# Optimization experiments

Hardware: AMD Instinct MI355X
Metric: run time of the kernel (lower is better)

Reference implementation:

```python
import jax, jax.numpy as jnp
import numpy as np

N = 100000  # nodes
E = 3200000  # edges
NEG_SLOPE = 0.2  # GATConv default


def _gat_conv(x, src, dst, edge_attr, W, a_src, a_dst, W_e, a_e, bias):
    """PyG GATConv, heads=1, concat=True, add_self_loops=True (fill_value='mean')."""
    n = x.shape[0]
    loop = jnp.arange(n)
    s = jnp.concatenate([src, loop])
    d = jnp.concatenate([dst, loop])
    mean_ea = edge_attr.mean(axis=0)
    ea = jnp.concatenate([edge_attr, jnp.broadcast_to(mean_ea, (n, edge_attr.shape[1]))], axis=0)
    h = x @ W                          # [N, C]
    al_src = h @ a_src                 # [N]
    al_dst = h @ a_dst                 # [N]
    he = ea @ W_e                      # [E+N, C]
    alpha = al_src[s] + al_dst[d] + he @ a_e   # [E+N]
    alpha = jax.nn.leaky_relu(alpha, NEG_SLOPE)
    amax = jax.ops.segment_max(alpha, d, num_segments=n)
    ex = jnp.exp(alpha - amax[d])
    denom = jax.ops.segment_sum(ex, d, num_segments=n)
    coef = ex / (denom[d] + 1e-16)     # per-destination softmax (PyG softmax)
    out = jax.ops.segment_sum(h[s] * coef[:, None], d, num_segments=n)
    return out + bias


def _edge_mlp(z, w0, b0, w1, b1, w2, b2, w3, b3):
    z = jax.nn.relu(z @ w0 + b0)
    z = jax.nn.relu(z @ w1 + b1)
    z = jax.nn.relu(z @ w2 + b2)
    return z @ w3 + b3


def setup_inputs() -> dict:
    key = jax.random.key(0)
    ks = jax.random.split(key, 24)
    g = lambda i, sh, s=0.1: jax.random.normal(ks[i], sh, dtype=jnp.float32) * s
    return {
        "x": g(0, (N, 4), 1.0),
        "edge_attr": g(1, (E, 3), 1.0),
        "W1": g(2, (4, 16), 0.5), "as1": g(3, (16,)), "ad1": g(4, (16,)),
        "We1": g(5, (3, 16), 0.5), "ae1": g(6, (16,)), "b1": g(7, (16,)),
        "mw0": g(8, (35, 16), 0.17), "mb0": g(9, (16,)),
        "mw1": g(10, (16, 16), 0.25), "mb1": g(11, (16,)),
        "mw2": g(12, (16, 8), 0.25), "mb2": g(13, (8,)),
        "mw3": g(14, (8, 4), 0.35), "mb3": g(15, (4,)),
        "W2": g(16, (16, 2), 0.25), "as2": g(17, (2,)), "ad2": g(18, (2,)),
        "We2": g(19, (4, 2), 0.5), "ae2": g(20, (2,)), "b2": g(21, (2,)),
        "edge_index": jax.random.randint(ks[22], (2, E), 0, N),
    }


def reference(x, edge_attr, W1, as1, ad1, We1, ae1, b1,
              mw0, mb0, mw1, mb1, mw2, mb2, mw3, mb3,
              W2, as2, ad2, We2, ae2, b2, edge_index):
    src, dst = edge_index[0], edge_index[1]
    h = _gat_conv(x, src, dst, edge_attr, W1, as1, ad1, We1, ae1, b1)      # [N, 16]
    z = jnp.concatenate([h[src], edge_attr, h[dst]], axis=1)               # [E, 35]
    e = _edge_mlp(z, mw0, mb0, mw1, mb1, mw2, mb2, mw3, mb3)               # [E, 4]
    out = _gat_conv(h, src, dst, e, W2, as2, ad2, We2, ae2, b2)            # [N, 2]
    return jax.nn.log_softmax(out, axis=1), jax.nn.log_softmax(e, axis=1)
```

## Files before the change

### kernel.cpp

```cpp
#include <hip/hip_runtime.h>
#include <hip/hip_bf16.h>
#include <stdint.h>

typedef __hip_bfloat16 bf16;
typedef unsigned long long ull;
#define NT 256
#define EPT 4

__device__ __forceinline__ float b2f(bf16 v){ return __bfloat162float(v); }
__device__ __forceinline__ bf16 f2b(float v){ return __float2bfloat16(v); }
__device__ __forceinline__ float lrelu(float a){ return a>0.f ? a : 0.2f*a; }
__device__ __forceinline__ float sanf(float v){ return __builtin_isfinite(v) ? v : -12345.f; }
__device__ __forceinline__ float us2f(unsigned short u){ return __uint_as_float(((unsigned)u)<<16); }
__device__ __forceinline__ unsigned short f2bu(float v){ bf16 b=f2b(v); unsigned short u; __builtin_memcpy(&u,&b,2); return u; }

__device__ __forceinline__ float ld(const void* p, size_t i, int f32in){
  return f32in ? ((const float*)p)[i] : b2f(((const bf16*)p)[i]);
}

__device__ __forceinline__ float waveReduceSum(float v){
#pragma unroll
  for(int o=32;o>0;o>>=1) v += __shfl_down(v,o,64);
  return v;
}

__device__ __forceinline__ unsigned clampi(int v, int n){
  unsigned u=(unsigned)v; return (u<(unsigned)n)?u:0u;
}

__device__ __forceinline__ void load_h1v(const bf16* h1, unsigned node, float* dst){
  const ull* p=(const ull*)(h1+(size_t)node*16);
#pragma unroll
  for(int q=0;q<4;q++){
    ull v=p[q];
    dst[q*4+0]=us2f((unsigned short)v);        dst[q*4+1]=us2f((unsigned short)(v>>16));
    dst[q*4+2]=us2f((unsigned short)(v>>32));  dst[q*4+3]=us2f((unsigned short)(v>>48));
  }
}
__device__ __forceinline__ void load_x4(const void* x, unsigned n, int f32in, float* o){
  if(f32in){ float4 v=((const float4*)x)[n]; o[0]=v.x;o[1]=v.y;o[2]=v.z;o[3]=v.w; }
  else{
    ull v=((const ull*)x)[n];
    o[0]=us2f((unsigned short)v);       o[1]=us2f((unsigned short)(v>>16));
    o[2]=us2f((unsigned short)(v>>32)); o[3]=us2f((unsigned short)(v>>48));
  }
}

__global__ __launch_bounds__(64) void k_probe(const unsigned short* __restrict__ xraw,
                                              int nscan, float* __restrict__ stats){
  int t=threadIdx.x;
  int bad=0;
  for(int k=t*8;k<t*8+8;k++){
    if(k<nscan){
      unsigned short u=xraw[k];
      unsigned ex=(u>>7)&0xFF;
      bool plaus = (ex==0u) || (ex>=97u && ex<=157u);
      if(!plaus) bad++;
    }
  }
#pragma unroll
  for(int o=32;o>0;o>>=1) bad += __shfl_down(bad,o,64);
  if(t==0){
    for(int i=0;i<7;i++) stats[i]=0.f;
    ((int*)stats)[7] = (bad>=8) ? 1 : 0;
  }
}

__global__ __launch_bounds__(NT) void k_prep(const void* __restrict__ ea,
                                             const int* __restrict__ idx,
                                             int* __restrict__ rowc,
                                             float* __restrict__ stats, int E, int N){
  const int f32in=((const int*)stats)[7];
  __shared__ float lds[16];
  float s0=0.f,s1=0.f,s2=0.f;
  for(size_t e=(size_t)blockIdx.x*NT+threadIdx.x; e<(size_t)E; e+=(size_t)gridDim.x*NT){
    s0+=ld(ea,e*3+0,f32in); s1+=ld(ea,e*3+1,f32in); s2+=ld(ea,e*3+2,f32in);
    unsigned d=clampi(idx[(size_t)E+e],N);
    atomicAdd(&rowc[d],1);
  }
  int lane=threadIdx.x&63, wv=threadIdx.x>>6;
  s0=waveReduceSum(s0); s1=waveReduceSum(s1); s2=waveReduceSum(s2);
  if(lane==0){ lds[wv*4+0]=s0; lds[wv*4+1]=s1; lds[wv*4+2]=s2; }
  __syncthreads();
  if(threadIdx.x==0){
    float a0=0,a1=0,a2=0;
    for(int w=0;w<NT/64;w++){ a0+=lds[w*4]; a1+=lds[w*4+1]; a2+=lds[w*4+2]; }
    atomicAdd(&stats[0],a0); atomicAdd(&stats[1],a1); atomicAdd(&stats[2],a2);
  }
}

__global__ __launch_bounds__(NT) void k_node1(
    const void* __restrict__ x, const void* __restrict__ W1,
    const void* __restrict__ as1, const void* __restrict__ ad1,
    const float* __restrict__ stats,
    float* __restrict__ als, float* __restrict__ ald, int N){
  const int f32in=((const int*)stats)[7];
  __shared__ float sW1[64], sas[16], sad[16];
  if(threadIdx.x<64) sW1[threadIdx.x]=ld(W1,threadIdx.x,f32in);
  if(threadIdx.x<16){ sas[threadIdx.x]=ld(as1,threadIdx.x,f32in); sad[threadIdx.x]=ld(ad1,threadIdx.x,f32in); }
  __syncthreads();
  int i=blockIdx.x*NT+threadIdx.x;
  if(i>=N) return;
  float xv[4]; load_x4(x,(unsigned)i,f32in,xv);
  float a_s=0.f,a_d=0.f;
#pragma unroll
  for(int j=0;j<16;j++){
    float v=xv[0]*sW1[j]+xv[1]*sW1[16+j]+xv[2]*sW1[32+j]+xv[3]*sW1[48+j];
    a_s+=v*sas[j]; a_d+=v*sad[j];
  }
  als[i]=a_s; ald[i]=a_d;
}

__global__ __launch_bounds__(NT) void k_scan1(const int* __restrict__ rowc, int* __restrict__ bsum, int N){
  __shared__ int sm[NT];
  int i=blockIdx.x*NT+threadIdx.x;
  sm[threadIdx.x]=(i<N)?rowc[i]:0;
  __syncthreads();
  for(int o=NT/2;o>0;o>>=1){ if(threadIdx.x<o) sm[threadIdx.x]+=sm[threadIdx.x+o]; __syncthreads(); }
  if(threadIdx.x==0) bsum[blockIdx.x]=sm[0];
}
__global__ __launch_bounds__(1024) void k_scan2(int* __restrict__ bsum, int NB){
  __shared__ int sm[1024];
  int i=threadIdx.x;
  int v=(i<NB)?bsum[i]:0;
  sm[i]=v; __syncthreads();
  for(int o=1;o<1024;o<<=1){
    int t=(i>=o)?sm[i-o]:0; __syncthreads();
    sm[i]+=t; __syncthreads();
  }
  if(i<NB) bsum[i]=(i==0)?0:sm[i-1];
}
__global__ __launch_bounds__(NT) void k_scan3(int* __restrict__ rowc, const int* __restrict__ bsum, int N){
  __shared__ int sm[NT];
  int i=blockIdx.x*NT+threadIdx.x;
  int v=(i<N)?rowc[i]:0;
  sm[threadIdx.x]=v; __syncthreads();
  for(int o=1;o<NT;o<<=1){
    int t=(threadIdx.x>=o)?sm[threadIdx.x-o]:0; __syncthreads();
    sm[threadIdx.x]+=t; __syncthreads();
  }
  if(i<N) rowc[i]=bsum[blockIdx.x]+sm[threadIdx.x]-v;
}

__global__ __launch_bounds__(NT) void k_scatter(
    const int* __restrict__ idx, const void* __restrict__ ea,
    const void* __restrict__ We1, const void* __restrict__ ae1,
    const float* __restrict__ als, const float* __restrict__ stats,
    int* __restrict__ rowc, ull* __restrict__ csr, int E, int N){
  const int f32in=((const int*)stats)[7];
  __shared__ float sve[3];
  if(threadIdx.x<3){
    float v=0.f;
    for(int j=0;j<16;j++) v+=ld(We1,threadIdx.x*16+j,f32in)*ld(ae1,j,f32in);
    sve[threadIdx.x]=v;
  }
  __syncthreads();
  int e=blockIdx.x*NT+threadIdx.x;
  if(e>=E) return;
  unsigned s=clampi(idx[e],N), d=clampi(idx[(size_t)E+e],N);
  float ap = als[s] + ld(ea,(size_t)e*3+0,f32in)*sve[0]
                    + ld(ea,(size_t)e*3+1,f32in)*sve[1]
                    + ld(ea,(size_t)e*3+2,f32in)*sve[2];
  int pos=atomicAdd(&rowc[d],1);
  csr[pos] = (ull)s | ((ull)__float_as_uint(ap)<<32);
}

__global__ __launch_bounds__(NT) void k_gather1(
    const ull* __restrict__ csr, const int* __restrict__ rowe,
    const float* __restrict__ als, const float* __restrict__ ald,
    const void* __restrict__ x, const void* __restrict__ W1, const void* __restrict__ b1,
    const void* __restrict__ W2, const void* __restrict__ as2, const void* __restrict__ ad2,
    const void* __restrict__ We1, const void* __restrict__ ae1,
    const float* __restrict__ stats, float invE,
    bf16* __restrict__ h1, float* __restrict__ h2,
    float* __restrict__ als2, float* __restrict__ ald2, int N){
  const int f32in=((const int*)stats)[7];
  __shared__ float sW1[64], sb1[16], sW2[32], sas2[2], sad2[2], saea[1];
  if(threadIdx.x<64) sW1[threadIdx.x]=ld(W1,threadIdx.x,f32in);
  if(threadIdx.x<16) sb1[threadIdx.x]=ld(b1,threadIdx.x,f32in);
  if(threadIdx.x<32) sW2[threadIdx.x]=ld(W2,threadIdx.x,f32in);
  if(threadIdx.x<2){ sas2[threadIdx.x]=ld(as2,threadIdx.x,f32in); sad2[threadIdx.x]=ld(ad2,threadIdx.x,f32in); }
  if(threadIdx.x==0){
    float a=0.f;
    for(int k=0;k<3;k++){
      float v=0.f;
      for(int j=0;j<16;j++) v+=ld(We1,k*16+j,f32in)*ld(ae1,j,f32in);
      a+=stats[k]*v;
    }
    saea[0]=a*invE;
  }
  __syncthreads();
  int n=blockIdx.x*16+(threadIdx.x>>4);
  int c=threadIdx.x&15;
  if(n>=N) return;
  int end=rowe[n];
  int start=(n==0)?0:rowe[n-1];
  float aldn=ald[n], alsn=als[n];
  float aself=lrelu(alsn+aldn+saea[0]);
  float w0=sW1[c], w1=sW1[16+c], w2=sW1[32+c], w3=sW1[48+c];
  float m=aself;
  for(int k=start+c;k<end;k+=16){
    float ap=__uint_as_float((unsigned)(csr[k]>>32));
    m=fmaxf(m,lrelu(ap+aldn));
  }
#pragma unroll
  for(int o=1;o<16;o<<=1) m=fmaxf(m,__shfl_xor(m,o,64));
  float xv[4]; load_x4(x,(unsigned)n,f32in,xv);
  float hc_self=xv[0]*w0+xv[1]*w1+xv[2]*w2+xv[3]*w3;
  float exs=expf(fminf(aself-m,0.f));
  float den=exs, acc=exs*hc_self;
  for(int k=start;k<end;k++){
    ull v=csr[k];
    unsigned src=(unsigned)(v&0xffffffffu);
    float ap=__uint_as_float((unsigned)(v>>32));
    float ex=expf(fminf(lrelu(ap+aldn)-m,0.f));
    den+=ex;
    float xs[4]; load_x4(x,src,f32in,xs);
    float hc=xs[0]*w0+xs[1]*w1+xs[2]*w2+xs[3]*w3;
    acc+=ex*hc;
  }
  float inv=1.f/(den+1e-16f);
  float h1c=acc*inv+sb1[c];
  h1[(size_t)n*16+c]=f2b(h1c);
  float r0=h1c*sW2[c*2+0], r1=h1c*sW2[c*2+1];
#pragma unroll
  for(int o=1;o<16;o<<=1){ r0+=__shfl_xor(r0,o,64); r1+=__shfl_xor(r1,o,64); }
  if(c==0){
    h2[(size_t)n*2+0]=r0; h2[(size_t)n*2+1]=r1;
    als2[n]=r0*sas2[0]+r1*sas2[1];
    ald2[n]=r0*sad2[0]+r1*sad2[1];
  }
}

__global__ __launch_bounds__(NT) void k_wprep(
    const void* mw0,const void* mb0,const void* mw1,const void* mb1,
    const void* mw2,const void* mb2,const void* mw3,const void* mb3,
    const void* We2,const void* ae2,
    const float* __restrict__ stats, float* __restrict__ gw){
  const int f32in=((const int*)stats)[7];
  for(int t=threadIdx.x;t<560;t+=NT) gw[t]=ld(mw0,t,f32in);
  for(int t=threadIdx.x;t<256;t+=NT) gw[576+t]=ld(mw1,t,f32in);
  for(int t=threadIdx.x;t<128;t+=NT) gw[848+t]=ld(mw2,t,f32in);
  if(threadIdx.x<32) gw[984+threadIdx.x]=ld(mw3,threadIdx.x,f32in);
  if(threadIdx.x<16){ gw[560+threadIdx.x]=ld(mb0,threadIdx.x,f32in); gw[832+threadIdx.x]=ld(mb1,threadIdx.x,f32in); }
  if(threadIdx.x<8) gw[976+threadIdx.x]=ld(mb2,threadIdx.x,f32in);
  if(threadIdx.x<4){
    gw[1016+threadIdx.x]=ld(mb3,threadIdx.x,f32in);
    gw[1020+threadIdx.x]=ld(We2,threadIdx.x*2+0,f32in)*ld(ae2,0,f32in)
                        +ld(We2,threadIdx.x*2+1,f32in)*ld(ae2,1,f32in);
  }
}

__global__ __launch_bounds__(NT) void k_upre(
    const bf16* __restrict__ h1, const float* __restrict__ gw,
    float* __restrict__ us, float* __restrict__ ud, int N){
  int n=blockIdx.x*NT+threadIdx.x;
  if(n>=N) return;
  float h[16]; load_h1v(h1,(unsigned)n,h);
  const float4* w4=(const float4*)gw;
  float4 a0,a1,a2,a3;
  { const float4* b=(const float4*)(gw+560); a0=b[0]; a1=b[1]; a2=b[2]; a3=b[3]; }
#pragma unroll
  for(int i=0;i<16;i++){
    float z=h[i];
    float4 r0=w4[i*4+0],r1=w4[i*4+1],r2=w4[i*4+2],r3=w4[i*4+3];
    a0.x+=z*r0.x; a0.y+=z*r0.y; a0.z+=z*r0.z; a0.w+=z*r0.w;
    a1.x+=z*r1.x; a1.y+=z*r1.y; a1.z+=z*r1.z; a1.w+=z*r1.w;
    a2.x+=z*r2.x; a2.y+=z*r2.y; a2.z+=z*r2.z; a2.w+=z*r2.w;
    a3.x+=z*r3.x; a3.y+=z*r3.y; a3.z+=z*r3.z; a3.w+=z*r3.w;
  }
  float4* po=(float4*)(us+(size_t)n*16);
  po[0]=a0; po[1]=a1; po[2]=a2; po[3]=a3;
  float4 c0=make_float4(0,0,0,0), c1=c0, c2=c0, c3=c0;
#pragma unroll
  for(int i=0;i<16;i++){
    float z=h[i];
    int r=19+i;
    float4 r0=w4[r*4+0],r1=w4[r*4+1],r2=w4[r*4+2],r3=w4[r*4+3];
    c0.x+=z*r0.x; c0.y+=z*r0.y; c0.z+=z*r0.z; c0.w+=z*r0.w;
    c1.x+=z*r1.x; c1.y+=z*r1.y; c1.z+=z*r1.z; c1.w+=z*r1.w;
    c2.x+=z*r2.x; c2.y+=z*r2.y; c2.z+=z*r2.z; c2.w+=z*r2.w;
    c3.x+=z*r3.x; c3.y+=z*r3.y; c3.z+=z*r3.z; c3.w+=z*r3.w;
  }
  float4* pd=(float4*)(ud+(size_t)n*16);
  pd[0]=c0; pd[1]=c1; pd[2]=c2; pd[3]=c3;
}

__device__ __forceinline__ void mlp_tail4(float t1[EPT][16],
                                          const float* __restrict__ gw,
                                          float ev[EPT][4]){
#pragma unroll
  for(int u=0;u<EPT;u++)
#pragma unroll
    for(int j=0;j<16;j++) t1[u][j]=fmaxf(t1[u][j],0.f);

  const float4* w14=(const float4*)(gw+576);
  float t2[EPT][16];
  {
    const float4* b=(const float4*)(gw+832);
    float4 b0=b[0],b1=b[1],b2=b[2],b3=b[3];
#pragma unroll
    for(int u=0;u<EPT;u++){
      t2[u][0]=b0.x; t2[u][1]=b0.y; t2[u][2]=b0.z; t2[u][3]=b0.w;
      t2[u][4]=b1.x; t2[u][5]=b1.y; t2[u][6]=b1.z; t2[u][7]=b1.w;
      t2[u][8]=b2.x; t2[u][9]=b2.y; t2[u][10]=b2.z; t2[u][11]=b2.w;
      t2[u][12]=b3.x; t2[u][13]=b3.y; t2[u][14]=b3.z; t2[u][15]=b3.w;
    }
  }
#pragma unroll
  for(int i2=0;i2<16;i2++){
    float4 r0=w14[i2*4+0], r1=w14[i2*4+1], r2=w14[i2*4+2], r3=w14[i2*4+3];
#pragma unroll
    for(int u=0;u<EPT;u++){
      float a=t1[u][i2];
      t2[u][0]+=a*r0.x; t2[u][1]+=a*r0.y; t2[u][2]+=a*r0.z; t2[u][3]+=a*r0.w;
      t2[u][4]+=a*r1.x; t2[u][5]+=a*r1.y; t2[u][6]+=a*r1.z; t2[u][7]+=a*r1.w;
      t2[u][8]+=a*r2.x; t2[u][9]+=a*r2.y; t2[u][10]+=a*r2.z; t2[u][11]+=a*r2.w;
      t2[u][12]+=a*r3.x; t2[u][13]+=a*r3.y; t2[u][14]+=a*r3.z; t2[u][15]+=a*r3.w;
    }
  }
#pragma unroll
  for(int u=0;u<EPT;u++)
#pragma unroll
    for(int j=0;j<16;j++) t2[u][j]=fmaxf(t2[u][j],0.f);

  const float4* w24=(const float4*)(gw+848);
  float t3[EPT][8];
  {
    const float4* b=(const float4*)(gw+976);
    float4 b0=b[0],b1=b[1];
#pragma unroll
    for(int u=0;u<EPT;u++){
      t3[u][0]=b0.x; t3[u][1]=b0.y; t3[u][2]=b0.z; t3[u][3]=b0.w;
      t3[u][4]=b1.x; t3[u][5]=b1.y; t3[u][6]=b1.z; t3[u][7]=b1.w;
    }
  }
#pragma unroll
  for(int i2=0;i2<16;i2++){
    float4 r0=w24[i2*2+0], r1=w24[i2*2+1];
#pragma unroll
    for(int u=0;u<EPT;u++){
      float a=t2[u][i2];
      t3[u][0]+=a*r0.x; t3[u][1]+=a*r0.y; t3[u][2]+=a*r0.z; t3[u][3]+=a*r0.w;
      t3[u][4]+=a*r1.x; t3[u][5]+=a*r1.y; t3[u][6]+=a*r1.z; t3[u][7]+=a*r1.w;
    }
  }
#pragma unroll
  for(int u=0;u<EPT;u++)
#pragma unroll
    for(int j=0;j<8;j++) t3[u][j]=fmaxf(t3[u][j],0.f);

  const float4* w34=(const float4*)(gw+984);
  {
    const float4* b=(const float4*)(gw+1016);
    float4 b0=b[0];
#pragma unroll
    for(int u=0;u<EPT;u++){ ev[u][0]=b0.x; ev[u][1]=b0.y; ev[u][2]=b0.z; ev[u][3]=b0.w; }
  }
#pragma unroll
  for(int i2=0;i2<8;i2++){
    float4 r0=w34[i2];
#pragma unroll
    for(int u=0;u<EPT;u++){
      float a=t3[u][i2];
      ev[u][0]+=a*r0.x; ev[u][1]+=a*r0.y; ev[u][2]+=a*r0.z; ev[u][3]+=a*r0.w;
    }
  }
}

__device__ __forceinline__ void mlp_head_full4(const float z[EPT][35],
                                               const float* __restrict__ gw,
                                               float t1[EPT][16]){
  const float4* w4=(const float4*)gw;
  {
    const float4* b=(const float4*)(gw+560);
    float4 b0=b[0],b1=b[1],b2=b[2],b3=b[3];
#pragma unroll
    for(int u=0;u<EPT;u++){
      t1[u][0]=b0.x; t1[u][1]=b0.y; t1[u][2]=b0.z; t1[u][3]=b0.w;
      t1[u][4]=b1.x; t1[u][5]=b1.y; t1[u][6]=b1.z; t1[u][7]=b1.w;
      t1[u][8]=b2.x; t1[u][9]=b2.y; t1[u][10]=b2.z; t1[u][11]=b2.w;
      t1[u][12]=b3.x; t1[u][13]=b3.y; t1[u][14]=b3.z; t1[u][15]=b3.w;
    }
  }
#pragma unroll
  for(int i2=0;i2<35;i2++){
    float4 r0=w4[i2*4+0], r1=w4[i2*4+1], r2=w4[i2*4+2], r3=w4[i2*4+3];
#pragma unroll
    for(int u=0;u<EPT;u++){
      float a=z[u][i2];
      t1[u][0]+=a*r0.x; t1[u][1]+=a*r0.y; t1[u][2]+=a*r0.z; t1[u][3]+=a*r0.w;
      t1[u][4]+=a*r1.x; t1[u][5]+=a*r1.y; t1[u][6]+=a*r1.z; t1[u][7]+=a*r1.w;
      t1[u][8]+=a*r2.x; t1[u][9]+=a*r2.y; t1[u][10]+=a*r2.z; t1[u][11]+=a*r2.w;
      t1[u][12]+=a*r3.x; t1[u][13]+=a*r3.y; t1[u][14]+=a*r3.z; t1[u][15]+=a*r3.w;
    }
  }
}

__device__ __forceinline__ void edge_epi(const float* ev, unsigned s, unsigned d, int e,
                                         const float* __restrict__ gw,
                                         const float* __restrict__ als2,
                                         const float* __restrict__ ald2,
                                         const float* __restrict__ h2,
                                         float* __restrict__ denom2, float* __restrict__ acc2,
                                         void* __restrict__ d_out, int f32in, int N){
  float m=fmaxf(fmaxf(ev[0],ev[1]),fmaxf(ev[2],ev[3]));
  float lse=m+logf(expf(ev[0]-m)+expf(ev[1]-m)+expf(ev[2]-m)+expf(ev[3]-m));
  if(f32in){
    float4 o; o.x=sanf(ev[0]-lse); o.y=sanf(ev[1]-lse); o.z=sanf(ev[2]-lse); o.w=sanf(ev[3]-lse);
    ((float4*)((float*)d_out+(size_t)2*N))[e]=o;
  }else{
    ull o = (ull)f2bu(sanf(ev[0]-lse))
          | ((ull)f2bu(sanf(ev[1]-lse))<<16)
          | ((ull)f2bu(sanf(ev[2]-lse))<<32)
          | ((ull)f2bu(sanf(ev[3]-lse))<<48);
    ((ull*)((bf16*)d_out+(size_t)2*N))[e]=o;
  }
  const float* s_ve2=gw+1020;
  float adot=ev[0]*s_ve2[0]+ev[1]*s_ve2[1]+ev[2]*s_ve2[2]+ev[3]*s_ve2[3];
  float a2=sanf(lrelu(als2[s]+ald2[d]+adot));
  float ex=expf(fminf(a2,80.f));
  float2 h2s=((const float2*)h2)[s];
  atomicAdd(&denom2[d],ex);
  atomicAdd(&acc2[(size_t)d*2+0],ex*h2s.x);
  atomicAdd(&acc2[(size_t)d*2+1],ex*h2s.y);
}

__device__ __forceinline__ void stats_red(float c0,float c1,float c2,float c3,
                                          float* s_red, float* stats){
  int lane=threadIdx.x&63, wv=threadIdx.x>>6;
  c0=waveReduceSum(c0); c1=waveReduceSum(c1); c2=waveReduceSum(c2); c3=waveReduceSum(c3);
  __syncthreads();
  if(lane==0){ s_red[wv*4]=c0; s_red[wv*4+1]=c1; s_red[wv*4+2]=c2; s_red[wv*4+3]=c3; }
  __syncthreads();
  if(threadIdx.x==0){
    float a0=0,a1=0,a2=0,a3=0;
    for(int w=0;w<NT/64;w++){ a0+=s_red[w*4]; a1+=s_red[w*4+1]; a2+=s_red[w*4+2]; a3+=s_red[w*4+3]; }
    atomicAdd(&stats[3],a0); atomicAdd(&stats[4],a1); atomicAdd(&stats[5],a2); atomicAdd(&stats[6],a3);
  }
}

__global__ __launch_bounds__(NT,2) void k_edge2s(
    const int* __restrict__ idx, const void* __restrict__ ea,
    const float* __restrict__ us, const float* __restrict__ ud,
    const float* __restrict__ als2, const float* __restrict__ ald2,
    const float* __restrict__ gw,
    const float* __restrict__ h2,
    float* __restrict__ denom2, float* __restrict__ acc2,
    float* __restrict__ stats, void* __restrict__ d_out, int E, int N){
  const int f32in=((const int*)stats)[7];
  __shared__ float s_red[16];
  size_t base=(size_t)blockIdx.x*(NT*EPT)+threadIdx.x;
  int e[EPT]; bool v[EPT]; int es[EPT]; unsigned s[EPT], d[EPT];
#pragma unroll
  for(int u=0;u<EPT;u++){
    e[u]=(int)(base+(size_t)u*NT);
    v[u]=e[u]<E;
    es[u]=v[u]?e[u]:0;
    s[u]=clampi(idx[es[u]],N);
    d[u]=clampi(idx[(size_t)E+es[u]],N);
  }
  float t1[EPT][16];
#pragma unroll
  for(int u=0;u<EPT;u++){
    const float4* p=(const float4*)(us+(size_t)s[u]*16);
    float4 a0=p[0],a1=p[1],a2=p[2],a3=p[3];
    t1[u][0]=a0.x; t1[u][1]=a0.y; t1[u][2]=a0.z; t1[u][3]=a0.w;
    t1[u][4]=a1.x; t1[u][5]=a1.y; t1[u][6]=a1.z; t1[u][7]=a1.w;
    t1[u][8]=a2.x; t1[u][9]=a2.y; t1[u][10]=a2.z; t1[u][11]=a2.w;
    t1[u][12]=a3.x; t1[u][13]=a3.y; t1[u][14]=a3.z; t1[u][15]=a3.w;
  }
  {
    const float4* w16=(const float4*)(gw+256);
    const float4* w17=(const float4*)(gw+272);
    const float4* w18=(const float4*)(gw+288);
    float4 q0[3]={w16[0],w17[0],w18[0]}, q1[3]={w16[1],w17[1],w18[1]},
           q2[3]={w16[2],w17[2],w18[2]}, q3[3]={w16[3],w17[3],w18[3]};
#pragma unroll
    for(int u=0;u<EPT;u++){
      float e3[3];
      e3[0]=ld(ea,(size_t)es[u]*3+0,f32in);
      e3[1]=ld(ea,(size_t)es[u]*3+1,f32in);
      e3[2]=ld(ea,(size_t)es[u]*3+2,f32in);
#pragma unroll
      for(int k=0;k<3;k++){
        float a=e3[k];
        t1[u][0]+=a*q0[k].x; t1[u][1]+=a*q0[k].y; t1[u][2]+=a*q0[k].z; t1[u][3]+=a*q0[k].w;
        t1[u][4]+=a*q1[k].x; t1[u][5]+=a*q1[k].y; t1[u][6]+=a*q1[k].z; t1[u][7]+=a*q1[k].w;
        t1[u][8]+=a*q2[k].x; t1[u][9]+=a*q2[k].y; t1[u][10]+=a*q2[k].z; t1[u][11]+=a*q2[k].w;
        t1[u][12]+=a*q3[k].x; t1[u][13]+=a*q3[k].y; t1[u][14]+=a*q3[k].z; t1[u][15]+=a*q3[k].w;
      }
    }
  }
#pragma unroll
  for(int u=0;u<EPT;u++){
    const float4* p=(const float4*)(ud+(size_t)d[u]*16);
    float4 a0=p[0],a1=p[1],a2=p[2],a3=p[3];
    t1[u][0]+=a0.x; t1[u][1]+=a0.y; t1[u][2]+=a0.z; t1[u][3]+=a0.w;
    t1[u][4]+=a1.x; t1[u][5]+=a1.y; t1[u][6]+=a1.z; t1[u][7]+=a1.w;
    t1[u][8]+=a2.x; t1[u][9]+=a2.y; t1[u][10]+=a2.z; t1[u][11]+=a2.w;
    t1[u][12]+=a3.x; t1[u][13]+=a3.y; t1[u][14]+=a3.z; t1[u][15]+=a3.w;
  }
  float ev[EPT][4];
  mlp_tail4(t1,gw,ev);
  float c0=0.f,c1=0.f,c2=0.f,c3=0.f;
#pragma unroll
  for(int u=0;u<EPT;u++){
    if(v[u]){
      edge_epi(ev[u],s[u],d[u],e[u],gw,als2,ald2,h2,denom2,acc2,d_out,f32in,N);
      c0+=ev[u][0]; c1+=ev[u][1]; c2+=ev[u][2]; c3+=ev[u][3];
    }
  }
  stats_red(c0,c1,c2,c3,s_red,stats);
}

__global__ __launch_bounds__(NT,1) void k_edge2(
    const int* __restrict__ idx, const void* __restrict__ ea,
    const bf16* __restrict__ h1,
    const float* __restrict__ als2, const float* __restrict__ ald2,
    const float* __restrict__ gw,
    const float* __restrict__ h2,
    float* __restrict__ denom2, float* __restrict__ acc2,
    float* __restrict__ stats, void* __restrict__ d_out, int E, int N){
  const int f32in=((const int*)stats)[7];
  __shared__ float s_red[16];
  size_t base=(size_t)blockIdx.x*(NT*EPT)+threadIdx.x;
  int e[EPT]; bool v[EPT]; int es[EPT]; unsigned s[EPT], d[EPT];
#pragma unroll
  for(int u=0;u<EPT;u++){
    e[u]=(int)(base+(size_t)u*NT);
    v[u]=e[u]<E;
    es[u]=v[u]?e[u]:0;
    s[u]=clampi(idx[es[u]],N);
    d[u]=clampi(idx[(size_t)E+es[u]],N);
  }
  float z[EPT][35];
#pragma unroll
  for(int u=0;u<EPT;u++){
    load_h1v(h1,s[u],z[u]);
    load_h1v(h1,d[u],z[u]+19);
    z[u][16]=ld(ea,(size_t)es[u]*3+0,f32in);
    z[u][17]=ld(ea,(size_t)es[u]*3+1,f32in);
    z[u][18]=ld(ea,(size_t)es[u]*3+2,f32in);
  }
  float t1[EPT][16];
  mlp_head_full4(z,gw,t1);
  float ev[EPT][4];
  mlp_tail4(t1,gw,ev);
  float c0=0.f,c1=0.f,c2=0.f,c3=0.f;
#pragma unroll
  for(int u=0;u<EPT;u++){
    if(v[u]){
      edge_epi(ev[u],s[u],d[u],e[u],gw,als2,ald2,h2,denom2,acc2,d_out,f32in,N);
      c0+=ev[u][0]; c1+=ev[u][1]; c2+=ev[u][2]; c3+=ev[u][3];
    }
  }
  stats_red(c0,c1,c2,c3,s_red,stats);
}

__global__ __launch_bounds__(NT) void k_final(
    const float* __restrict__ stats, float invE,
    const float* __restrict__ als2, const float* __restrict__ ald2,
    const void* __restrict__ We2, const void* __restrict__ ae2,
    const float* __restrict__ h2,
    const float* __restrict__ denom2, const float* __restrict__ acc2,
    const void* __restrict__ bias2, void* __restrict__ d_out, int N){
  const int f32in=((const int*)stats)[7];
  __shared__ float s_ve2[4], s_b2[2];
  if(threadIdx.x<4)
    s_ve2[threadIdx.x]=ld(We2,threadIdx.x*2+0,f32in)*ld(ae2,0,f32in)
                      +ld(We2,threadIdx.x*2+1,f32in)*ld(ae2,1,f32in);
  if(threadIdx.x<2) s_b2[threadIdx.x]=ld(bias2,threadIdx.x,f32in);
  __syncthreads();
  int i=blockIdx.x*NT+threadIdx.x;
  if(i>=N) return;
  float adot=(stats[3]*s_ve2[0]+stats[4]*s_ve2[1]+stats[5]*s_ve2[2]+stats[6]*s_ve2[3])*invE;
  float self=lrelu(als2[i]+ald2[i]+adot);
  float ex=expf(fminf(self,80.f));
  float den=denom2[i]+ex;
  float inv=1.f/(den+1e-16f);
  float o0=(acc2[(size_t)i*2+0]+ex*h2[(size_t)i*2+0])*inv+s_b2[0];
  float o1=(acc2[(size_t)i*2+1]+ex*h2[(size_t)i*2+1])*inv+s_b2[1];
  float m=fmaxf(o0,o1);
  float lse=m+logf(expf(o0-m)+expf(o1-m));
  float r0=sanf(o0-lse), r1=sanf(o1-lse);
  if(f32in){
    float* o=(float*)d_out;
    o[(size_t)i*2+0]=r0; o[(size_t)i*2+1]=r1;
  }else{
    bf16* o=(bf16*)d_out;
    o[(size_t)i*2+0]=f2b(r0); o[(size_t)i*2+1]=f2b(r1);
  }
}

extern "C" void kernel_launch(void* const* d_in, const int* in_sizes, int n_in,
                              void* d_out, int out_size, void* d_ws, size_t ws_size,
                              hipStream_t stream){
  const void* x   =d_in[0];
  const void* ea  =d_in[1];
  const void* W1  =d_in[2];
  const void* as1 =d_in[3];
  const void* ad1 =d_in[4];
  const void* We1 =d_in[5];
  const void* ae1 =d_in[6];
  const void* b1  =d_in[7];
  const void* mw0 =d_in[8];
  const void* mb0 =d_in[9];
  const void* mw1 =d_in[10];
  const void* mb1 =d_in[11];
  const void* mw2 =d_in[12];
  const void* mb2 =d_in[13];
  const void* mw3 =d_in[14];
  const void* mb3 =d_in[15];
  const void* W2  =d_in[16];
  const void* as2 =d_in[17];
  const void* ad2 =d_in[18];
  const void* We2 =d_in[19];
  const void* ae2 =d_in[20];
  const void* bias2=d_in[21];
  const int*  idx =(const int*)d_in[22];

  int N=in_sizes[0]/4;
  int E=in_sizes[1]/3;
  float invE=1.f/(float)E;

  float*    F     =(float*)d_ws;
  float*    stats =F;
  float*    als   =F+8;
  float*    ald   =als+N;
  float*    ald2  =ald+N;
  int*      rowc  =(int*)(ald2+N);
  bf16*     h1    =(bf16*)(rowc+N);
  float*    h2    =(float*)(h1+(size_t)16*N);
  float*    acc2  =h2+(size_t)2*N;
  float*    den2  =ald;
  float*    gw    =(float*)((((uintptr_t)rowc)+15)&~(uintptr_t)15);
  float*    u_s   =(float*)((((uintptr_t)(acc2+(size_t)2*N))+15)&~(uintptr_t)15);
  float*    u_d   =u_s+(size_t)16*N;
  size_t    need  =(size_t)((char*)(u_d+(size_t)16*N)-(char*)d_ws);
  int use_split   =(ws_size>=need)?1:0;

  ull* csr =(ull*)((char*)d_out+(size_t)4*N);
  int* bsum=(int*)((char*)d_out+(size_t)4*N);

  int NBn=(N+NT-1)/NT, nbE=(E+NT-1)/NT;
  int nbE4=(E+NT*EPT-1)/(NT*EPT);
  int nscan=in_sizes[0]*2; if(nscan>512) nscan=512;

  hipMemsetAsync(rowc,0,(size_t)N*sizeof(int),stream);
  k_probe  <<<1,64,0,stream>>>((const unsigned short*)x,nscan,stats);
  k_prep   <<<1024,NT,0,stream>>>(ea,idx,rowc,stats,E,N);
  k_node1  <<<NBn,NT,0,stream>>>(x,W1,as1,ad1,stats,als,ald,N);
  k_scan1  <<<NBn,NT,0,stream>>>(rowc,bsum,N);
  k_scan2  <<<1,1024,0,stream>>>(bsum,NBn);
  k_scan3  <<<NBn,NT,0,stream>>>(rowc,bsum,N);
  k_scatter<<<nbE,NT,0,stream>>>(idx,ea,We1,ae1,als,stats,rowc,csr,E,N);
  k_gather1<<<(N+15)/16,NT,0,stream>>>(csr,rowc,als,ald,x,W1,b1,W2,as2,ad2,We1,ae1,
                                       stats,invE,h1,h2,als,ald2,N);
  k_wprep  <<<1,NT,0,stream>>>(mw0,mb0,mw1,mb1,mw2,mb2,mw3,mb3,We2,ae2,stats,gw);
  hipMemsetAsync(den2,0,(size_t)N*sizeof(float),stream);
  hipMemsetAsync(acc2,0,(size_t)2*N*sizeof(float),stream);
  if(use_split){
    k_upre   <<<NBn,NT,0,stream>>>(h1,gw,u_s,u_d,N);
    k_edge2s <<<nbE4,NT,0,stream>>>(idx,ea,u_s,u_d,als,ald2,gw,h2,den2,acc2,stats,d_out,E,N);
  }else{
    k_edge2  <<<nbE4,NT,0,stream>>>(idx,ea,h1,als,ald2,gw,h2,den2,acc2,stats,d_out,E,N);
  }
  k_final  <<<NBn,NT,0,stream>>>(stats,invE,als,ald2,We2,ae2,h2,den2,acc2,bias2,d_out,N);
}
```

Measured before the change: 1.134 ms.

## Use a wavefront per node in gather1 and fewer edges per thread in edge2s

```diff
diff --git a/kernel.cpp b/kernel.cpp
--- a/kernel.cpp
+++ b/kernel.cpp
@@ -6,6 +6,7 @@
 typedef unsigned long long ull;
 #define NT 256
 #define EPT 4
+#define EPTS 2
 
 __device__ __forceinline__ float b2f(bf16 v){ return __bfloat162float(v); }
 __device__ __forceinline__ bf16 f2b(float v){ return __float2bfloat16(v); }
@@ -190,42 +191,45 @@
     saea[0]=a*invE;
   }
   __syncthreads();
-  int n=blockIdx.x*16+(threadIdx.x>>4);
-  int c=threadIdx.x&15;
+  int wv=threadIdx.x>>6, lane=threadIdx.x&63;
+  int n=blockIdx.x*4+wv;
   if(n>=N) return;
+  int c=lane&15, sg=lane>>4;
   int end=rowe[n];
   int start=(n==0)?0:rowe[n-1];
   float aldn=ald[n], alsn=als[n];
   float aself=lrelu(alsn+aldn+saea[0]);
   float w0=sW1[c], w1=sW1[16+c], w2=sW1[32+c], w3=sW1[48+c];
   float m=aself;
-  for(int k=start+c;k<end;k+=16){
+  for(int k=start+lane;k<end;k+=64){
     float ap=__uint_as_float((unsigned)(csr[k]>>32));
     m=fmaxf(m,lrelu(ap+aldn));
   }
 #pragma unroll
-  for(int o=1;o<16;o<<=1) m=fmaxf(m,__shfl_xor(m,o,64));
+  for(int o=1;o<64;o<<=1) m=fmaxf(m,__shfl_xor(m,o,64));
   float xv[4]; load_x4(x,(unsigned)n,f32in,xv);
   float hc_self=xv[0]*w0+xv[1]*w1+xv[2]*w2+xv[3]*w3;
   float exs=expf(fminf(aself-m,0.f));
-  float den=exs, acc=exs*hc_self;
-  for(int k=start;k<end;k++){
+  float den=0.f, acc=0.f;
+  for(int k=start+sg;k<end;k+=4){
     ull v=csr[k];
     unsigned src=(unsigned)(v&0xffffffffu);
     float ap=__uint_as_float((unsigned)(v>>32));
     float ex=expf(fminf(lrelu(ap+aldn)-m,0.f));
     den+=ex;
     float xs[4]; load_x4(x,src,f32in,xs);
-    float hc=xs[0]*w0+xs[1]*w1+xs[2]*w2+xs[3]*w3;
-    acc+=ex*hc;
-  }
+    acc+=ex*(xs[0]*w0+xs[1]*w1+xs[2]*w2+xs[3]*w3);
+  }
+  acc+=__shfl_xor(acc,16,64); acc+=__shfl_xor(acc,32,64);
+  den+=__shfl_xor(den,16,64); den+=__shfl_xor(den,32,64);
+  den+=exs; acc+=exs*hc_self;
   float inv=1.f/(den+1e-16f);
   float h1c=acc*inv+sb1[c];
-  h1[(size_t)n*16+c]=f2b(h1c);
+  if(sg==0) h1[(size_t)n*16+c]=f2b(h1c);
   float r0=h1c*sW2[c*2+0], r1=h1c*sW2[c*2+1];
 #pragma unroll
   for(int o=1;o<16;o<<=1){ r0+=__shfl_xor(r0,o,64); r1+=__shfl_xor(r1,o,64); }
-  if(c==0){
+  if(lane==0){
     h2[(size_t)n*2+0]=r0; h2[(size_t)n*2+1]=r1;
     als2[n]=r0*sas2[0]+r1*sas2[1];
     ald2[n]=r0*sad2[0]+r1*sad2[1];
@@ -286,21 +290,22 @@
   pd[0]=c0; pd[1]=c1; pd[2]=c2; pd[3]=c3;
 }
 
-__device__ __forceinline__ void mlp_tail4(float t1[EPT][16],
-                                          const float* __restrict__ gw,
-                                          float ev[EPT][4]){
-#pragma unroll
-  for(int u=0;u<EPT;u++)
+template<int EP>
+__device__ __forceinline__ void mlp_tail(float (&t1)[EP][16],
+                                         const float* __restrict__ gw,
+                                         float (&ev)[EP][4]){
+#pragma unroll
+  for(int u=0;u<EP;u++)
 #pragma unroll
     for(int j=0;j<16;j++) t1[u][j]=fmaxf(t1[u][j],0.f);
 
   const float4* w14=(const float4*)(gw+576);
-  float t2[EPT][16];
+  float t2[EP][16];
   {
     const float4* b=(const float4*)(gw+832);
     float4 b0=b[0],b1=b[1],b2=b[2],b3=b[3];
 #pragma unroll
-    for(int u=0;u<EPT;u++){
+    for(int u=0;u<EP;u++){
       t2[u][0]=b0.x; t2[u][1]=b0.y; t2[u][2]=b0.z; t2[u][3]=b0.w;
       t2[u][4]=b1.x; t2[u][5]=b1.y; t2[u][6]=b1.z; t2[u][7]=b1.w;
       t2[u][8]=b2.x; t2[u][9]=b2.y; t2[u][10]=b2.z; t2[u][11]=b2.w;
@@ -311,7 +316,7 @@
   for(int i2=0;i2<16;i2++){
     float4 r0=w14[i2*4+0], r1=w14[i2*4+1], r2=w14[i2*4+2], r3=w14[i2*4+3];
 #pragma unroll
-    for(int u=0;u<EPT;u++){
+    for(int u=0;u<EP;u++){
       float a=t1[u][i2];
       t2[u][0]+=a*r0.x; t2[u][1]+=a*r0.y; t2[u][2]+=a*r0.z; t2[u][3]+=a*r0.w;
       t2[u][4]+=a*r1.x; t2[u][5]+=a*r1.y; t2[u][6]+=a*r1.z; t2[u][7]+=a*r1.w;
@@ -320,17 +325,17 @@
     }
   }
 #pragma unroll
-  for(int u=0;u<EPT;u++)
+  for(int u=0;u<EP;u++)
 #pragma unroll
     for(int j=0;j<16;j++) t2[u][j]=fmaxf(t2[u][j],0.f);
 
   const float4* w24=(const float4*)(gw+848);
-  float t3[EPT][8];
+  float t3[EP][8];
   {
     const float4* b=(const float4*)(gw+976);
     float4 b0=b[0],b1=b[1];
 #pragma unroll
-    for(int u=0;u<EPT;u++){
+    for(int u=0;u<EP;u++){
       t3[u][0]=b0.x; t3[u][1]=b0.y; t3[u][2]=b0.z; t3[u][3]=b0.w;
       t3[u][4]=b1.x; t3[u][5]=b1.y; t3[u][6]=b1.z; t3[u][7]=b1.w;
     }
@@ -339,14 +344,14 @@
   for(int i2=0;i2<16;i2++){
     float4 r0=w24[i2*2+0], r1=w24[i2*2+1];
 #pragma unroll
-    for(int u=0;u<EPT;u++){
+    for(int u=0;u<EP;u++){
       float a=t2[u][i2];
       t3[u][0]+=a*r0.x; t3[u][1]+=a*r0.y; t3[u][2]+=a*r0.z; t3[u][3]+=a*r0.w;
       t3[u][4]+=a*r1.x; t3[u][5]+=a*r1.y; t3[u][6]+=a*r1.z; t3[u][7]+=a*r1.w;
     }
   }
 #pragma unroll
-  for(int u=0;u<EPT;u++)
+  for(int u=0;u<EP;u++)
 #pragma unroll
     for(int j=0;j<8;j++) t3[u][j]=fmaxf(t3[u][j],0.f);
 
@@ -355,13 +360,13 @@
     const float4* b=(const float4*)(gw+1016);
     float4 b0=b[0];
 #pragma unroll
-    for(int u=0;u<EPT;u++){ ev[u][0]=b0.x; ev[u][1]=b0.y; ev[u][2]=b0.z; ev[u][3]=b0.w; }
+    for(int u=0;u<EP;u++){ ev[u][0]=b0.x; ev[u][1]=b0.y; ev[u][2]=b0.z; ev[u][3]=b0.w; }
   }
 #pragma unroll
   for(int i2=0;i2<8;i2++){
     float4 r0=w34[i2];
 #pragma unroll
-    for(int u=0;u<EPT;u++){
+    for(int u=0;u<EP;u++){
       float a=t3[u][i2];
       ev[u][0]+=a*r0.x; ev[u][1]+=a*r0.y; ev[u][2]+=a*r0.z; ev[u][3]+=a*r0.w;
     }
@@ -370,7 +375,7 @@
 
 __device__ __forceinline__ void mlp_head_full4(const float z[EPT][35],
                                                const float* __restrict__ gw,
-                                               float t1[EPT][16]){
+                                               float (&t1)[EPT][16]){
   const float4* w4=(const float4*)gw;
   {
     const float4* b=(const float4*)(gw+560);
@@ -440,7 +445,7 @@
   }
 }
 
-__global__ __launch_bounds__(NT,2) void k_edge2s(
+__global__ __launch_bounds__(NT) void k_edge2s(
     const int* __restrict__ idx, const void* __restrict__ ea,
     const float* __restrict__ us, const float* __restrict__ ud,
     const float* __restrict__ als2, const float* __restrict__ ald2,
@@ -450,19 +455,19 @@
     float* __restrict__ stats, void* __restrict__ d_out, int E, int N){
   const int f32in=((const int*)stats)[7];
   __shared__ float s_red[16];
-  size_t base=(size_t)blockIdx.x*(NT*EPT)+threadIdx.x;
-  int e[EPT]; bool v[EPT]; int es[EPT]; unsigned s[EPT], d[EPT];
-#pragma unroll
-  for(int u=0;u<EPT;u++){
+  size_t base=(size_t)blockIdx.x*(NT*EPTS)+threadIdx.x;
+  int e[EPTS]; bool v[EPTS]; int es[EPTS]; unsigned s[EPTS], d[EPTS];
+#pragma unroll
+  for(int u=0;u<EPTS;u++){
     e[u]=(int)(base+(size_t)u*NT);
     v[u]=e[u]<E;
     es[u]=v[u]?e[u]:0;
     s[u]=clampi(idx[es[u]],N);
     d[u]=clampi(idx[(size_t)E+es[u]],N);
   }
-  float t1[EPT][16];
-#pragma unroll
-  for(int u=0;u<EPT;u++){
+  float t1[EPTS][16];
+#pragma unroll
+  for(int u=0;u<EPTS;u++){
     const float4* p=(const float4*)(us+(size_t)s[u]*16);
     float4 a0=p[0],a1=p[1],a2=p[2],a3=p[3];
     t1[u][0]=a0.x; t1[u][1]=a0.y; t1[u][2]=a0.z; t1[u][3]=a0.w;
@@ -477,7 +482,7 @@
     float4 q0[3]={w16[0],w17[0],w18[0]}, q1[3]={w16[1],w17[1],w18[1]},
            q2[3]={w16[2],w17[2],w18[2]}, q3[3]={w16[3],w17[3],w18[3]};
 #pragma unroll
-    for(int u=0;u<EPT;u++){
+    for(int u=0;u<EPTS;u++){
       float e3[3];
       e3[0]=ld(ea,(size_t)es[u]*3+0,f32in);
       e3[1]=ld(ea,(size_t)es[u]*3+1,f32in);
@@ -493,7 +498,7 @@
     }
   }
 #pragma unroll
-  for(int u=0;u<EPT;u++){
+  for(int u=0;u<EPTS;u++){
     const float4* p=(const float4*)(ud+(size_t)d[u]*16);
     float4 a0=p[0],a1=p[1],a2=p[2],a3=p[3];
     t1[u][0]+=a0.x; t1[u][1]+=a0.y; t1[u][2]+=a0.z; t1[u][3]+=a0.w;
@@ -501,11 +506,11 @@
     t1[u][8]+=a2.x; t1[u][9]+=a2.y; t1[u][10]+=a2.z; t1[u][11]+=a2.w;
     t1[u][12]+=a3.x; t1[u][13]+=a3.y; t1[u][14]+=a3.z; t1[u][15]+=a3.w;
   }
-  float ev[EPT][4];
-  mlp_tail4(t1,gw,ev);
+  float ev[EPTS][4];
+  mlp_tail<EPTS>(t1,gw,ev);
   float c0=0.f,c1=0.f,c2=0.f,c3=0.f;
 #pragma unroll
-  for(int u=0;u<EPT;u++){
+  for(int u=0;u<EPTS;u++){
     if(v[u]){
       edge_epi(ev[u],s[u],d[u],e[u],gw,als2,ald2,h2,denom2,acc2,d_out,f32in,N);
       c0+=ev[u][0]; c1+=ev[u][1]; c2+=ev[u][2]; c3+=ev[u][3];
@@ -546,7 +551,7 @@
   float t1[EPT][16];
   mlp_head_full4(z,gw,t1);
   float ev[EPT][4];
-  mlp_tail4(t1,gw,ev);
+  mlp_tail<EPT>(t1,gw,ev);
   float c0=0.f,c1=0.f,c2=0.f,c3=0.f;
 #pragma unroll
   for(int u=0;u<EPT;u++){
@@ -645,6 +650,7 @@
 
   int NBn=(N+NT-1)/NT, nbE=(E+NT-1)/NT;
   int nbE4=(E+NT*EPT-1)/(NT*EPT);
+  int nbEs=(E+NT*EPTS-1)/(NT*EPTS);
   int nscan=in_sizes[0]*2; if(nscan>512) nscan=512;
 
   hipMemsetAsync(rowc,0,(size_t)N*sizeof(int),stream);
@@ -655,14 +661,14 @@
   k_scan2  <<<1,1024,0,stream>>>(bsum,NBn);
   k_scan3  <<<NBn,NT,0,stream>>>(rowc,bsum,N);
   k_scatter<<<nbE,NT,0,stream>>>(idx,ea,We1,ae1,als,stats,rowc,csr,E,N);
-  k_gather1<<<(N+15)/16,NT,0,stream>>>(csr,rowc,als,ald,x,W1,b1,W2,as2,ad2,We1,ae1,
-                                       stats,invE,h1,h2,als,ald2,N);
+  k_gather1<<<(N+3)/4,NT,0,stream>>>(csr,rowc,als,ald,x,W1,b1,W2,as2,ad2,We1,ae1,
+                                     stats,invE,h1,h2,als,ald2,N);
   k_wprep  <<<1,NT,0,stream>>>(mw0,mb0,mw1,mb1,mw2,mb2,mw3,mb3,We2,ae2,stats,gw);
   hipMemsetAsync(den2,0,(size_t)N*sizeof(float),stream);
   hipMemsetAsync(acc2,0,(size_t)2*N*sizeof(float),stream);
   if(use_split){
     k_upre   <<<NBn,NT,0,stream>>>(h1,gw,u_s,u_d,N);
-    k_edge2s <<<nbE4,NT,0,stream>>>(idx,ea,u_s,u_d,als,ald2,gw,h2,den2,acc2,stats,d_out,E,N);
+    k_edge2s <<<nbEs,NT,0,stream>>>(idx,ea,u_s,u_d,als,ald2,gw,h2,den2,acc2,stats,d_out,E,N);
   }else{
     k_edge2  <<<nbE4,NT,0,stream>>>(idx,ea,h1,als,ald2,gw,h2,den2,acc2,stats,d_out,E,N);
   }
```

Result: slower. 1.224 ms (+8.0%).
